# Optimization experiments

Measured on AMD Instinct MI355X. Metric: run time of the kernel, lower is better.

Reference implementation:

```python
import jax, jax.numpy as jnp
import numpy as np

V = 40000          # number of pillars
IN_C = 64          # pillar feature channels
OUT_C = 64         # conv output channels
X, Y = 512, 512    # BEV grid size
B = 4              # batch size


def setup_inputs() -> dict:
    key = jax.random.key(0)
    k1, k2, k3 = jax.random.split(key, 3)
    pillar_features = jax.random.normal(k1, (V, IN_C), dtype=jnp.float32)
    # which only matters on duplicates)
    flat = np.random.default_rng(0).choice(X * Y, size=V, replace=False)
    voxel_indices = jnp.asarray(np.stack([flat // Y, flat % Y], axis=1), dtype=jnp.int32)
    conv_w = jax.random.normal(k2, (OUT_C, IN_C), dtype=jnp.float32) * 0.05  # 1x1 conv kernel
    conv_b = jax.random.normal(k3, (OUT_C,), dtype=jnp.float32) * 0.05
    return {
        "pillar_features": pillar_features,
        "conv_w": conv_w,
        "conv_b": conv_b,
        "voxel_indices": voxel_indices,
        "batch_size": B,
    }


def reference(pillar_features, conv_w, conv_b, voxel_indices, batch_size):
    x = voxel_indices[:, 0]
    y = voxel_indices[:, 1]
    valid = (x >= 0) & (x < X) & (y >= 0) & (y < Y)
    # push invalid entries out of bounds and drop them in the scatter
    xs = jnp.where(valid, x, X)
    ys = jnp.where(valid, y, Y)
    # scatter pillar features into dense BEV canvas [X, Y, C]
    canvas = jnp.zeros((X, Y, IN_C), dtype=pillar_features.dtype)
    canvas = canvas.at[xs, ys].set(pillar_features, mode="drop")
    # 1x1 conv == per-cell matmul over channels; original code writes the same
    # canvas into every batch slice (mask is >= 0, not == b), so compute once
    bev = jnp.einsum("xyc,oc->oxy", canvas, conv_w) + conv_b[:, None, None]
    return jnp.broadcast_to(bev[None], (batch_size, OUT_C, X, Y))
```

## Files before the change

kernel.cpp:

```cpp
#include <hip/hip_runtime.h>
#include <hip/hip_bf16.h>


#define V_PILLARS 40000
#define XDIM 512
#define YDIM 512
#define C 64
#define BATCH 4

__global__ __launch_bounds__(256) void k_pillar_conv(
    const float* __restrict__ pf,
    const float* __restrict__ cw,
    const float* __restrict__ cb,
    const int*   __restrict__ vidx,
    int*   __restrict__ map,
    float* __restrict__ res)
{
    __shared__ float swt[64 * 68];
    const int t    = threadIdx.x;
    const int lane = t & 63;
    const int w    = t >> 6;

    for (int i = t; i < 64 * 16; i += 256) {
        const int o = i >> 4, j = i & 15;
        float4 v = ((const float4*)cw)[i];
        *((float4*)&swt[o * 68 + 4 * j]) = v;
    }
    __syncthreads();

    float4 wr[16];
#pragma unroll
    for (int j = 0; j < 16; j++)
        wr[j] = *((const float4*)&swt[lane * 68 + 4 * j]);
    const float bias = cb[lane];

    const int gw = blockIdx.x * 4 + w;
    const int nw = gridDim.x * 4;
    for (int p = gw; p < V_PILLARS; p += nw) {
        const float4* a4 = (const float4*)(pf + (size_t)p * C);
        float acc = bias;
#pragma unroll
        for (int j = 0; j < 16; j++) {
            const float4 a = a4[j];
            acc += a.x * wr[j].x + a.y * wr[j].y + a.z * wr[j].z + a.w * wr[j].w;
        }
        res[(size_t)p * C + lane] = acc;
        if (lane == 0) {
            const int xx = vidx[2 * p], yy = vidx[2 * p + 1];
            if (xx >= 0 && xx < XDIM && yy >= 0 && yy < YDIM)
                map[xx * YDIM + yy] = p;
        }
    }
}

__global__ __launch_bounds__(256) void k_write_out(
    const float* __restrict__ res,
    const float* __restrict__ cb,
    const int*   __restrict__ map,
    float*       __restrict__ out)
{
    __shared__ int   smap[64];
    __shared__ float sres[64][65];
    const int t    = threadIdx.x;
    const int lane = t & 63;
    const int w    = t >> 6;
    const int x  = (int)blockIdx.x >> 3;
    const int y0 = ((int)blockIdx.x & 7) << 6;

    if (t < 64) smap[t] = map[x * YDIM + y0 + t];
    const float bias = cb[lane];
    __syncthreads();

#pragma unroll
    for (int i = 0; i < 16; i++) {
        const int y = w * 16 + i;
        const int v = smap[y];
        float val;
        if (v >= 0) val = res[(size_t)v * C + lane];
        else        val = bias;
        sres[y][lane] = val;
    }
    __syncthreads();

    const size_t base = (size_t)x * YDIM + y0 + lane;
#pragma unroll
    for (int i = 0; i < 16; i++) {
        const int o = w * 16 + i;
        const float val = sres[lane][o];
        const size_t idx = (size_t)o * (XDIM * YDIM) + base;
        out[idx]                           = val;
        out[idx + 1u * C * XDIM * YDIM]    = val;
        out[idx + 2u * (size_t)C * XDIM * YDIM] = val;
        out[idx + 3u * (size_t)C * XDIM * YDIM] = val;
    }
}

extern "C" void kernel_launch(void* const* d_in, const int* in_sizes, int n_in,
                              void* d_out, int out_size, void* d_ws, size_t ws_size,
                              hipStream_t stream) {
    const float* pf   = (const float*)d_in[0];
    const float* cw   = (const float*)d_in[1];
    const float* cb   = (const float*)d_in[2];
    const int*   vidx = (const int*)d_in[3];
    float* out = (float*)d_out;

    int*   map = (int*)d_ws;
    float* res = (float*)((char*)d_ws + (1 << 20));

    hipMemsetAsync(map, 0xFF, XDIM * YDIM * sizeof(int), stream);

    k_pillar_conv<<<1024, 256, 0, stream>>>(pf, cw, cb, vidx, map, res);
    k_write_out<<<XDIM * (YDIM / 64), 256, 0, stream>>>(res, cb, map, out);
}
```

Before: 326.6 us.

## Fuse 1x1 conv into output-writing kernel and shrink index map to uint16

Splits the scatter into a tiny index-map kernel and moves the per-pillar 64x64 matvec into the output writer, so conv results are computed on the fly instead of staged through a workspace buffer. The index map drops to 16-bit entries, halving its memset and reads. Output stores become 16-byte vectorised nontemporal writes, with each thread writing four consecutive y values. The cost is that every output block now loads the weights into LDS and registers, and a 16-bit map limits the pillar count to under 65535.

```diff
diff --git a/kernel.cpp b/kernel.cpp
--- a/kernel.cpp
+++ b/kernel.cpp
@@ -1,5 +1,4 @@
 #include <hip/hip_runtime.h>
-#include <hip/hip_bf16.h>
 
 
 #define V_PILLARS 40000
@@ -7,19 +6,40 @@
 #define YDIM 512
 #define C 64
 #define BATCH 4
+#define PLANE (XDIM * YDIM)
 
-__global__ __launch_bounds__(256) void k_pillar_conv(
+typedef float f32x4 __attribute__((ext_vector_type(4)));
+
+__global__ __launch_bounds__(256) void k_scatter(
+    const int* __restrict__ vidx,
+    unsigned short* __restrict__ map)
+{
+    const int p = blockIdx.x * 256 + threadIdx.x;
+    if (p < V_PILLARS) {
+        const int2 xy = ((const int2*)vidx)[p];
+        if (xy.x >= 0 && xy.x < XDIM && xy.y >= 0 && xy.y < YDIM)
+            map[xy.x * YDIM + xy.y] = (unsigned short)p;
+    }
+}
+
+__global__ __launch_bounds__(256) void k_conv_write(
     const float* __restrict__ pf,
     const float* __restrict__ cw,
     const float* __restrict__ cb,
-    const int*   __restrict__ vidx,
-    int*   __restrict__ map,
-    float* __restrict__ res)
+    const unsigned short* __restrict__ map,
+    float* __restrict__ out)
 {
     __shared__ float swt[64 * 68];
+    __shared__ float sres[64][65];
+    __shared__ unsigned short smap[64];
+
     const int t    = threadIdx.x;
     const int lane = t & 63;
     const int w    = t >> 6;
+    const int x  = (int)blockIdx.x >> 3;
+    const int y0 = ((int)blockIdx.x & 7) << 6;
+
+    if (t < 64) smap[t] = map[x * YDIM + y0 + t];
 
     for (int i = t; i < 64 * 16; i += 256) {
         const int o = i >> 4, j = i & 15;
@@ -34,64 +54,40 @@
         wr[j] = *((const float4*)&swt[lane * 68 + 4 * j]);
     const float bias = cb[lane];
 
-    const int gw = blockIdx.x * 4 + w;
-    const int nw = gridDim.x * 4;
-    for (int p = gw; p < V_PILLARS; p += nw) {
-        const float4* a4 = (const float4*)(pf + (size_t)p * C);
-        float acc = bias;
-#pragma unroll
-        for (int j = 0; j < 16; j++) {
-            const float4 a = a4[j];
-            acc += a.x * wr[j].x + a.y * wr[j].y + a.z * wr[j].z + a.w * wr[j].w;
-        }
-        res[(size_t)p * C + lane] = acc;
-        if (lane == 0) {
-            const int xx = vidx[2 * p], yy = vidx[2 * p + 1];
-            if (xx >= 0 && xx < XDIM && yy >= 0 && yy < YDIM)
-                map[xx * YDIM + yy] = p;
-        }
-    }
-}
-
-__global__ __launch_bounds__(256) void k_write_out(
-    const float* __restrict__ res,
-    const float* __restrict__ cb,
-    const int*   __restrict__ map,
-    float*       __restrict__ out)
-{
-    __shared__ int   smap[64];
-    __shared__ float sres[64][65];
-    const int t    = threadIdx.x;
-    const int lane = t & 63;
-    const int w    = t >> 6;
-    const int x  = (int)blockIdx.x >> 3;
-    const int y0 = ((int)blockIdx.x & 7) << 6;
-
-    if (t < 64) smap[t] = map[x * YDIM + y0 + t];
-    const float bias = cb[lane];
-    __syncthreads();
-
 #pragma unroll
     for (int i = 0; i < 16; i++) {
         const int y = w * 16 + i;
         const int v = smap[y];
-        float val;
-        if (v >= 0) val = res[(size_t)v * C + lane];
-        else        val = bias;
-        sres[y][lane] = val;
+        float acc = bias;
+        if (v != 0xFFFF) {
+            const float4* a4 = (const float4*)(pf + (size_t)v * C);
+#pragma unroll
+            for (int j = 0; j < 16; j++) {
+                const float4 a = a4[j];
+                acc += a.x * wr[j].x + a.y * wr[j].y + a.z * wr[j].z + a.w * wr[j].w;
+            }
+        }
+        sres[y][lane] = acc;
     }
     __syncthreads();
 
-    const size_t base = (size_t)x * YDIM + y0 + lane;
+    const int o_sub = lane >> 4;
+    const int yq    = lane & 15;
+    const size_t ybase = (size_t)x * YDIM + y0 + 4 * yq;
 #pragma unroll
-    for (int i = 0; i < 16; i++) {
-        const int o = w * 16 + i;
-        const float val = sres[lane][o];
-        const size_t idx = (size_t)o * (XDIM * YDIM) + base;
-        out[idx]                           = val;
-        out[idx + 1u * C * XDIM * YDIM]    = val;
-        out[idx + 2u * (size_t)C * XDIM * YDIM] = val;
-        out[idx + 3u * (size_t)C * XDIM * YDIM] = val;
+    for (int it = 0; it < 4; it++) {
+        const int o = w * 16 + it * 4 + o_sub;
+        f32x4 val;
+        val.x = sres[4 * yq + 0][o];
+        val.y = sres[4 * yq + 1][o];
+        val.z = sres[4 * yq + 2][o];
+        val.w = sres[4 * yq + 3][o];
+        const size_t idx = (size_t)o * PLANE + ybase;
+#pragma unroll
+        for (int b = 0; b < BATCH; b++) {
+            __builtin_nontemporal_store(
+                val, (f32x4*)(out + idx + (size_t)b * C * PLANE));
+        }
     }
 }
 
@@ -104,11 +100,10 @@
     const int*   vidx = (const int*)d_in[3];
     float* out = (float*)d_out;
 
-    int*   map = (int*)d_ws;
-    float* res = (float*)((char*)d_ws + (1 << 20));
+    unsigned short* map = (unsigned short*)d_ws;
 
-    hipMemsetAsync(map, 0xFF, XDIM * YDIM * sizeof(int), stream);
+    hipMemsetAsync(map, 0xFF, PLANE * sizeof(unsigned short), stream);
 
-    k_pillar_conv<<<1024, 256, 0, stream>>>(pf, cw, cb, vidx, map, res);
-    k_write_out<<<XDIM * (YDIM / 64), 256, 0, stream>>>(res, cb, map, out);
+    k_scatter<<<(V_PILLARS + 255) / 256, 256, 0, stream>>>(vidx, map);
+    k_conv_write<<<XDIM * (YDIM / 64), 256, 0, stream>>>(pf, cw, cb, map, out);
 }
```

Result: no change. 332.7 us (+1.9%).
